# Performance work log

Hardware: AMD Instinct MI355X
Metric: run time of the kernel (lower is better)

Reference implementation:

```python
import jax, jax.numpy as jnp
import numpy as np

N_HEADS = 16
K = 8
DILATION = 2
EPS = 1e-6
SCALE = 1.0  # use_qk_norm=True, learn_qk_scale=False -> buffer scale = 1.0


def _dilated_mask(N):
    # allowed[i, j] = (|i-j| <= k*dilation) and ((i-j) % dilation == 0)
    i = jnp.arange(N)[:, None]
    j = jnp.arange(N)[None, :]
    diff = i - j
    return (jnp.abs(diff) <= K * DILATION) & (diff % DILATION == 0)


def setup_inputs() -> dict:
    key = jax.random.key(0)
    k1, k2, k3 = jax.random.split(key, 3)
    B, N, D = 2, 2048, 1024
    x = jax.random.normal(k1, (B, N, D), dtype=jnp.float32)
    w_qkv = jax.random.normal(k2, (3 * D, D), dtype=jnp.float32) * (1.0 / np.sqrt(D))
    b_qkv = jnp.zeros((3 * D,), dtype=jnp.float32)
    w_out = jax.random.normal(k3, (D, D), dtype=jnp.float32) * (1.0 / np.sqrt(D))
    b_out = jnp.zeros((D,), dtype=jnp.float32)
    return {"x": x, "w_qkv": w_qkv, "b_qkv": b_qkv, "w_out": w_out, "b_out": b_out}


def reference(x, w_qkv, b_qkv, w_out, b_out):
    B, N, D = x.shape
    H = N_HEADS
    dh = D // H

    qkv = x @ w_qkv.T + b_qkv                      # [B, N, 3D]
    q, k, v = jnp.split(qkv, 3, axis=-1)
    # [B, N, D] -> [B, H, N, dh]
    q = q.reshape(B, N, H, dh).transpose(0, 2, 1, 3)
    k = k.reshape(B, N, H, dh).transpose(0, 2, 1, 3)
    v = v.reshape(B, N, H, dh).transpose(0, 2, 1, 3)

    # QK-norm
    q = q / (jnp.linalg.norm(q, axis=-1, keepdims=True) + EPS)
    k = k / (jnp.linalg.norm(k, axis=-1, keepdims=True) + EPS)

    scores = jnp.einsum('bhnd,bhmd->bhnm', q, k) * SCALE  # [B, H, N, N]
    allowed = _dilated_mask(N)                              # [N, N] bool
    scores = jnp.where(allowed, scores, -jnp.inf)
    attn = jax.nn.softmax(scores, axis=-1)

    out = jnp.einsum('bhnm,bhmd->bhnd', attn, v)            # [B, H, N, dh]
    out = out.transpose(0, 2, 1, 3).reshape(B, N, D)
    return out @ w_out.T + b_out
```

## Files before the change

kernel.cpp:

```cpp
#include <hip/hip_runtime.h>
#include <hip/hip_bf16.h>
#include <math.h>

typedef __bf16 bf16x8 __attribute__((ext_vector_type(8)));
typedef __bf16 bf16x4 __attribute__((ext_vector_type(4)));
typedef float f32x4 __attribute__((ext_vector_type(4)));

#define TM 128
#define BK 64


__device__ inline void async16(const void* g, void* l) {
    __builtin_amdgcn_global_load_lds(
        (const __attribute__((address_space(1))) unsigned int*)g,
        (__attribute__((address_space(3))) unsigned int*)l, 16, 0, 0);
}

__device__ inline void stage_sw(__bf16* S, const __bf16* G, int row0, int K, int k0,
                                int tid, int nchunks) {
#pragma unroll
    for (int ci = tid; ci < nchunks; ci += 256) {
        const int r  = ci >> 3;
        const int c  = ci & 7;
        const int cg = c ^ (r & 7);
        const char* g = (const char*)G + ((size_t)(row0 + r) * K + k0 + cg * 8) * 2;
        async16(g, (char*)S + ci * 16);
    }
}

__device__ inline bf16x8 frag_sw(const __bf16* S, int r, int cfrag) {
    const int c = cfrag ^ (r & 7);
    return *(const bf16x8*)(S + r * 64 + c * 8);
}

__global__ __launch_bounds__(256) void split_mat(
    const float* __restrict__ s0, __bf16* __restrict__ h0, __bf16* __restrict__ l0, int n0,
    const float* __restrict__ s1, __bf16* __restrict__ h1, __bf16* __restrict__ l1, int n1,
    const float* __restrict__ s2, __bf16* __restrict__ h2, __bf16* __restrict__ l2, int n2)
{
    const float* s; __bf16* h; __bf16* l; int n;
    if (blockIdx.y == 0)      { s = s0; h = h0; l = l0; n = n0; }
    else if (blockIdx.y == 1) { s = s1; h = h1; l = l1; n = n1; }
    else                      { s = s2; h = h2; l = l2; n = n2; }
    const int base = (blockIdx.x * 256 + threadIdx.x) * 8;
    if (base >= n) return;

    float buf[8];
    if (blockIdx.y == 2) {
#pragma unroll
        for (int m = 0; m < 8; m++) {
            const int p   = base + m;
            const int src = (p & ~63) + (((p & 63) >> 2) + 16 * (p & 3));
            buf[m] = s[src];
        }
    } else {
        float4 a = ((const float4*)(s + base))[0];
        float4 b = ((const float4*)(s + base))[1];
        buf[0] = a.x; buf[1] = a.y; buf[2] = a.z; buf[3] = a.w;
        buf[4] = b.x; buf[5] = b.y; buf[6] = b.z; buf[7] = b.w;
    }

    bf16x8 hv, lv;
#pragma unroll
    for (int j = 0; j < 8; j++) {
        __bf16 hb = (__bf16)buf[j];
        hv[j] = hb;
        lv[j] = (__bf16)(buf[j] - (float)hb);
    }
    *(bf16x8*)(h + base) = hv;
    if (l) *(bf16x8*)(l + base) = lv;
}

__global__ __launch_bounds__(256) void gemm_qkv(
    const __bf16* __restrict__ A, const __bf16* __restrict__ W,
    const float* __restrict__ bias,
    __bf16* __restrict__ q, __bf16* __restrict__ k, __bf16* __restrict__ v,
    int M, int N, int K)
{
    __shared__ __bf16 sA[TM * BK];
    __shared__ __bf16 sW[TM * BK];

    const int tid  = threadIdx.x;
    const int lane = tid & 63;
    const int wave = tid >> 6;
    const int bm = blockIdx.y * TM;
    const int bn = blockIdx.x * 128;
    const int wm = (wave >> 1) * 64;
    const int wn = (wave & 1) * 64;
    const int frow = lane & 15;

    f32x4 acc[4][4] = {};

    for (int k0 = 0; k0 < K; k0 += BK) {
        stage_sw(sA, A, bm, K, k0, tid, TM * 8);
        stage_sw(sW, W, bn, K, k0, tid, TM * 8);
        __syncthreads();

#pragma unroll
        for (int half = 0; half < 2; half++) {
            const int cf = half * 4 + (lane >> 4);
            bf16x8 aF[4], bF[4];
#pragma unroll
            for (int t = 0; t < 4; t++) {
                aF[t] = frag_sw(sA, wm + t * 16 + frow, cf);
                bF[t] = frag_sw(sW, wn + t * 16 + frow, cf);
            }
#pragma unroll
            for (int i = 0; i < 4; i++)
#pragma unroll
                for (int j = 0; j < 4; j++)
                    acc[i][j] = __builtin_amdgcn_mfma_f32_16x16x32_bf16(aF[i], bF[j], acc[i][j], 0, 0, 0);
        }
        __syncthreads();
    }

    const int col0 = bn + wn;
    const int t  = col0 >> 10;
    const int h  = (col0 & 1023) >> 6;

    float bv[4];
#pragma unroll
    for (int j = 0; j < 4; j++) bv[j] = bias[col0 + j * 16 + (lane & 15)];

    float inv_n[4][4];
    if (t < 2) {
#pragma unroll
        for (int i = 0; i < 4; i++)
#pragma unroll
            for (int r = 0; r < 4; r++) {
                float ss = 0.f;
#pragma unroll
                for (int j = 0; j < 4; j++) {
                    float val = acc[i][j][r] + bv[j];
                    ss = fmaf(val, val, ss);
                }
                ss += __shfl_xor(ss, 1);
                ss += __shfl_xor(ss, 2);
                ss += __shfl_xor(ss, 4);
                ss += __shfl_xor(ss, 8);
                inv_n[i][r] = 1.0f / (sqrtf(ss) + 1e-6f);
            }
    }

    __bf16* dstbase = (t == 0) ? q : (t == 1) ? k : v;
    const int c4 = (lane & 15) * 4;
#pragma unroll
    for (int i = 0; i < 4; i++) {
        const int gmBase = bm + wm + i * 16 + (lane >> 4) * 4;
#pragma unroll
        for (int r = 0; r < 4; r++) {
            const int gm = gmBase + r;
            bf16x4 ov;
#pragma unroll
            for (int j = 0; j < 4; j++) {
                float val = acc[i][j][r] + bv[j];
                if (t < 2) val *= inv_n[i][r];
                ov[j] = (__bf16)val;
            }
            const int b  = gm >> 11;
            const int ii = gm & 2047;
            *(bf16x4*)(dstbase + (((size_t)(b * 16 + h) * 2048) + ii) * 64 + c4) = ov;
        }
    }
}

__global__ __launch_bounds__(256) void gemm_out(
    const __bf16* __restrict__ A,
    const __bf16* __restrict__ Wh, const __bf16* __restrict__ Wl,
    const float* __restrict__ bias, float* __restrict__ C,
    int M, int N, int K)
{
    __shared__ __bf16 sA[TM * BK];
    __shared__ __bf16 sWh[64 * BK];
    __shared__ __bf16 sWl[64 * BK];

    const int tid  = threadIdx.x;
    const int lane = tid & 63;
    const int wave = tid >> 6;
    const int bm = blockIdx.y * TM;
    const int bn = blockIdx.x * 64;
    const int wm = (wave >> 1) * 64;
    const int wn = (wave & 1) * 32;
    const int frow = lane & 15;

    f32x4 acc[4][2] = {};

    for (int k0 = 0; k0 < K; k0 += BK) {
        stage_sw(sA,  A,  bm, K, k0, tid, TM * 8);
        stage_sw(sWh, Wh, bn, K, k0, tid, 64 * 8);
        stage_sw(sWl, Wl, bn, K, k0, tid, 64 * 8);
        __syncthreads();

#pragma unroll
        for (int half = 0; half < 2; half++) {
            const int cf = half * 4 + (lane >> 4);
            bf16x8 aH[4], bH[2], bL[2];
#pragma unroll
            for (int t = 0; t < 4; t++)
                aH[t] = frag_sw(sA, wm + t * 16 + frow, cf);
#pragma unroll
            for (int t = 0; t < 2; t++) {
                bH[t] = frag_sw(sWh, wn + t * 16 + frow, cf);
                bL[t] = frag_sw(sWl, wn + t * 16 + frow, cf);
            }
#pragma unroll
            for (int i = 0; i < 4; i++)
#pragma unroll
                for (int j = 0; j < 2; j++) {
                    acc[i][j] = __builtin_amdgcn_mfma_f32_16x16x32_bf16(aH[i], bH[j], acc[i][j], 0, 0, 0);
                    acc[i][j] = __builtin_amdgcn_mfma_f32_16x16x32_bf16(aH[i], bL[j], acc[i][j], 0, 0, 0);
                }
        }
        __syncthreads();
    }

#pragma unroll
    for (int i = 0; i < 4; i++) {
        const int gmBase = bm + wm + i * 16 + (lane >> 4) * 4;
#pragma unroll
        for (int j = 0; j < 2; j++) {
            const int gn = bn + wn + j * 16 + (lane & 15);
            const float bvj = bias[gn];
#pragma unroll
            for (int r = 0; r < 4; r++)
                C[(size_t)(gmBase + r) * N + gn] = acc[i][j][r] + bvj;
        }
    }
}

__global__ __launch_bounds__(256) void attn_sparse(
    const __bf16* __restrict__ q, const __bf16* __restrict__ k,
    const __bf16* __restrict__ v, __bf16* __restrict__ ao )
{
    const int wid  = blockIdx.x * 4 + (threadIdx.x >> 6);
    const int lane = threadIdx.x & 63;
    const int g    = lane >> 3;
    const int ld   = (lane & 7) * 8;

    const int bh = wid >> 8;
    const int i  = (wid & 255) * 8 + g;

    const __bf16* qb = q + (size_t)bh * 2048 * 64;
    const __bf16* kb = k + (size_t)bh * 2048 * 64;
    const __bf16* vb = v + (size_t)bh * 2048 * 64;

    bf16x8 qv = *(const bf16x8*)(qb + (size_t)i * 64 + ld);
    float qf[8];
#pragma unroll
    for (int e = 0; e < 8; e++) qf[e] = (float)qv[e];

    float s[17];
#pragma unroll
    for (int t = 0; t < 17; t++) {
        const int j = i + 2 * t - 16;
        const bool valid = (j >= 0) && (j < 2048);
        const int jc = valid ? j : i;
        bf16x8 kv = *(const bf16x8*)(kb + (size_t)jc * 64 + ld);
        float prod = qf[0] * (float)kv[0];
#pragma unroll
        for (int e = 1; e < 8; e++) prod = fmaf(qf[e], (float)kv[e], prod);
        prod += __shfl_xor(prod, 1);
        prod += __shfl_xor(prod, 2);
        prod += __shfl_xor(prod, 4);
        s[t] = valid ? prod : -INFINITY;
    }

    float m = s[0];
#pragma unroll
    for (int t = 1; t < 17; t++) m = fmaxf(m, s[t]);
    float denom = 0.f, p[17];
#pragma unroll
    for (int t = 0; t < 17; t++) { p[t] = __expf(s[t] - m); denom += p[t]; }
    const float inv = 1.0f / denom;

    float a[8] = {};
#pragma unroll
    for (int t = 0; t < 17; t++) {
        const int j = i + 2 * t - 16;
        const int jc = (j >= 0 && j < 2048) ? j : i;
        bf16x8 vv = *(const bf16x8*)(vb + (size_t)jc * 64 + ld);
#pragma unroll
        for (int e = 0; e < 8; e++) a[e] = fmaf(p[t], (float)vv[e], a[e]);
    }

    const int b = bh >> 4, h = bh & 15;
    bf16x8 o;
#pragma unroll
    for (int e = 0; e < 8; e++) o[e] = (__bf16)(a[e] * inv);
    *(bf16x8*)(ao + ((size_t)(b * 2048 + i)) * 1024 + h * 64 + ld) = o;
}

extern "C" void kernel_launch(void* const* d_in, const int* in_sizes, int n_in,
                              void* d_out, int out_size, void* d_ws, size_t ws_size,
                              hipStream_t stream)
{
    const float* x     = (const float*)d_in[0];
    const float* w_qkv = (const float*)d_in[1];
    const float* b_qkv = (const float*)d_in[2];
    const float* w_out = (const float*)d_in[3];
    const float* b_out = (const float*)d_in[4];
    float* out = (float*)d_out;

    const int Dn = 1024;
    const int M  = 4096;
    const int nx = 4194304, nwq = 3145728, nwo = 1048576;

    char* p = (char*)d_ws;
    __bf16* q   = (__bf16*)p;  p += (size_t)nx * 2;
    __bf16* kk  = (__bf16*)p;  p += (size_t)nx * 2;
    __bf16* vv  = (__bf16*)p;  p += (size_t)nx * 2;
    __bf16* xh  = (__bf16*)p;  p += (size_t)nx * 2;
    __bf16* wqh = (__bf16*)p;  p += (size_t)nwq * 2;
    __bf16* woh = (__bf16*)p;  p += (size_t)nwo * 2;
    __bf16* wol = (__bf16*)p;  p += (size_t)nwo * 2;
    __bf16* ao  = xh;

    {
        dim3 grid(nx / 8 / 256, 3);
        hipLaunchKernelGGL(split_mat, grid, dim3(256), 0, stream,
                           x, xh, (__bf16*)nullptr, nx,
                           w_qkv, wqh, (__bf16*)nullptr, nwq,
                           w_out, woh, wol, nwo);
    }
    {
        dim3 grid(3 * Dn / 128, M / TM);
        hipLaunchKernelGGL(gemm_qkv, grid, dim3(256), 0, stream,
                           xh, wqh, b_qkv, q, kk, vv, M, 3 * Dn, Dn);
    }
    hipLaunchKernelGGL(attn_sparse, dim3(2048), dim3(256), 0, stream,
                       q, kk, vv, ao);
    {
        dim3 grid(Dn / 64, M / TM);
        hipLaunchKernelGGL(gemm_out, grid, dim3(256), 0, stream,
                           ao, woh, wol, b_out, out, M, Dn, Dn);
    }
}
```

Baseline: 168.6 us.

## Double-buffer LDS tiles in QKV and output GEMMs with halved K step

```diff
diff --git a/kernel.cpp b/kernel.cpp
--- a/kernel.cpp
+++ b/kernel.cpp
@@ -7,7 +7,7 @@
 typedef float f32x4 __attribute__((ext_vector_type(4)));
 
 #define TM 128
-#define BK 64
+#define BK 32
 
 
 __device__ inline void async16(const void* g, void* l) {
@@ -20,17 +20,17 @@
                                 int tid, int nchunks) {
 #pragma unroll
     for (int ci = tid; ci < nchunks; ci += 256) {
-        const int r  = ci >> 3;
-        const int c  = ci & 7;
-        const int cg = c ^ (r & 7);
+        const int r  = ci >> 2;
+        const int c  = ci & 3;
+        const int cg = c ^ (r & 3);
         const char* g = (const char*)G + ((size_t)(row0 + r) * K + k0 + cg * 8) * 2;
         async16(g, (char*)S + ci * 16);
     }
 }
 
 __device__ inline bf16x8 frag_sw(const __bf16* S, int r, int cfrag) {
-    const int c = cfrag ^ (r & 7);
-    return *(const bf16x8*)(S + r * 64 + c * 8);
+    const int c = cfrag ^ (r & 3);
+    return *(const bf16x8*)(S + r * 32 + c * 8);
 }
 
 __global__ __launch_bounds__(256) void split_mat(
@@ -77,8 +77,8 @@
     __bf16* __restrict__ q, __bf16* __restrict__ k, __bf16* __restrict__ v,
     int M, int N, int K)
 {
-    __shared__ __bf16 sA[TM * BK];
-    __shared__ __bf16 sW[TM * BK];
+    __shared__ __bf16 sA[2][TM * BK];
+    __shared__ __bf16 sW[2][TM * BK];
 
     const int tid  = threadIdx.x;
     const int lane = tid & 63;
@@ -88,30 +88,33 @@
     const int wm = (wave >> 1) * 64;
     const int wn = (wave & 1) * 64;
     const int frow = lane & 15;
+    const int cf   = lane >> 4;
 
     f32x4 acc[4][4] = {};
 
+    stage_sw(sA[0], A, bm, K, 0, tid, TM * 4);
+    stage_sw(sW[0], W, bn, K, 0, tid, TM * 4);
+    __syncthreads();
+
+    int cur = 0;
     for (int k0 = 0; k0 < K; k0 += BK) {
-        stage_sw(sA, A, bm, K, k0, tid, TM * 8);
-        stage_sw(sW, W, bn, K, k0, tid, TM * 8);
+        if (k0 + BK < K) {
+            stage_sw(sA[cur ^ 1], A, bm, K, k0 + BK, tid, TM * 4);
+            stage_sw(sW[cur ^ 1], W, bn, K, k0 + BK, tid, TM * 4);
+        }
+        bf16x8 aF[4], bF[4];
+#pragma unroll
+        for (int t = 0; t < 4; t++) {
+            aF[t] = frag_sw(sA[cur], wm + t * 16 + frow, cf);
+            bF[t] = frag_sw(sW[cur], wn + t * 16 + frow, cf);
+        }
+#pragma unroll
+        for (int i = 0; i < 4; i++)
+#pragma unroll
+            for (int j = 0; j < 4; j++)
+                acc[i][j] = __builtin_amdgcn_mfma_f32_16x16x32_bf16(aF[i], bF[j], acc[i][j], 0, 0, 0);
         __syncthreads();
-
-#pragma unroll
-        for (int half = 0; half < 2; half++) {
-            const int cf = half * 4 + (lane >> 4);
-            bf16x8 aF[4], bF[4];
-#pragma unroll
-            for (int t = 0; t < 4; t++) {
-                aF[t] = frag_sw(sA, wm + t * 16 + frow, cf);
-                bF[t] = frag_sw(sW, wn + t * 16 + frow, cf);
-            }
-#pragma unroll
-            for (int i = 0; i < 4; i++)
-#pragma unroll
-                for (int j = 0; j < 4; j++)
-                    acc[i][j] = __builtin_amdgcn_mfma_f32_16x16x32_bf16(aF[i], bF[j], acc[i][j], 0, 0, 0);
-        }
-        __syncthreads();
+        cur ^= 1;
     }
 
     const int col0 = bn + wn;
@@ -170,9 +173,9 @@
     const float* __restrict__ bias, float* __restrict__ C,
     int M, int N, int K)
 {
-    __shared__ __bf16 sA[TM * BK];
-    __shared__ __bf16 sWh[64 * BK];
-    __shared__ __bf16 sWl[64 * BK];
+    __shared__ __bf16 sA[2][TM * BK];
+    __shared__ __bf16 sWh[2][64 * BK];
+    __shared__ __bf16 sWl[2][64 * BK];
 
     const int tid  = threadIdx.x;
     const int lane = tid & 63;
@@ -182,36 +185,40 @@
     const int wm = (wave >> 1) * 64;
     const int wn = (wave & 1) * 32;
     const int frow = lane & 15;
+    const int cf   = lane >> 4;
 
     f32x4 acc[4][2] = {};
 
+    stage_sw(sA[0],  A,  bm, K, 0, tid, TM * 4);
+    stage_sw(sWh[0], Wh, bn, K, 0, tid, 64 * 4);
+    stage_sw(sWl[0], Wl, bn, K, 0, tid, 64 * 4);
+    __syncthreads();
+
+    int cur = 0;
     for (int k0 = 0; k0 < K; k0 += BK) {
-        stage_sw(sA,  A,  bm, K, k0, tid, TM * 8);
-        stage_sw(sWh, Wh, bn, K, k0, tid, 64 * 8);
-        stage_sw(sWl, Wl, bn, K, k0, tid, 64 * 8);
+        if (k0 + BK < K) {
+            stage_sw(sA[cur ^ 1],  A,  bm, K, k0 + BK, tid, TM * 4);
+            stage_sw(sWh[cur ^ 1], Wh, bn, K, k0 + BK, tid, 64 * 4);
+            stage_sw(sWl[cur ^ 1], Wl, bn, K, k0 + BK, tid, 64 * 4);
+        }
+        bf16x8 aH[4], bH[2], bL[2];
+#pragma unroll
+        for (int t = 0; t < 4; t++)
+            aH[t] = frag_sw(sA[cur], wm + t * 16 + frow, cf);
+#pragma unroll
+        for (int t = 0; t < 2; t++) {
+            bH[t] = frag_sw(sWh[cur], wn + t * 16 + frow, cf);
+            bL[t] = frag_sw(sWl[cur], wn + t * 16 + frow, cf);
+        }
+#pragma unroll
+        for (int i = 0; i < 4; i++)
+#pragma unroll
+            for (int j = 0; j < 2; j++) {
+                acc[i][j] = __builtin_amdgcn_mfma_f32_16x16x32_bf16(aH[i], bH[j], acc[i][j], 0, 0, 0);
+                acc[i][j] = __builtin_amdgcn_mfma_f32_16x16x32_bf16(aH[i], bL[j], acc[i][j], 0, 0, 0);
+            }
         __syncthreads();
-
-#pragma unroll
-        for (int half = 0; half < 2; half++) {
-            const int cf = half * 4 + (lane >> 4);
-            bf16x8 aH[4], bH[2], bL[2];
-#pragma unroll
-            for (int t = 0; t < 4; t++)
-                aH[t] = frag_sw(sA, wm + t * 16 + frow, cf);
-#pragma unroll
-            for (int t = 0; t < 2; t++) {
-                bH[t] = frag_sw(sWh, wn + t * 16 + frow, cf);
-                bL[t] = frag_sw(sWl, wn + t * 16 + frow, cf);
-            }
-#pragma unroll
-            for (int i = 0; i < 4; i++)
-#pragma unroll
-                for (int j = 0; j < 2; j++) {
-                    acc[i][j] = __builtin_amdgcn_mfma_f32_16x16x32_bf16(aH[i], bH[j], acc[i][j], 0, 0, 0);
-                    acc[i][j] = __builtin_amdgcn_mfma_f32_16x16x32_bf16(aH[i], bL[j], acc[i][j], 0, 0, 0);
-                }
-        }
-        __syncthreads();
+        cur ^= 1;
     }
 
 #pragma unroll
```

Result: slower. 184.6 us (+9.5%).
